# Performance work log

Hardware: AMD Instinct MI355X
Metric: run time of the kernel (lower is better)

The kernel has to match this reference:

```python
import jax, jax.numpy as jnp
import numpy as np

P = 16
IMG_SIZES = [(512, 512), (512, 384), (448, 512), (384, 384), (320, 448), (256, 512), (384, 256), (512, 320)]
LMAX = 1024
B, DIM, HEADS, DH, DEPTH, MLP, NC = 8, 512, 8, 64, 6, 2048, 1000
PD = 3 * P * P  # 768 patch dim


def layer_norm(x, w, b=None, eps=1e-5):
    mu = x.mean(-1, keepdims=True)
    var = ((x - mu) ** 2).mean(-1, keepdims=True)
    y = (x - mu) * jax.lax.rsqrt(var + eps) * w
    return y + b if b is not None else y


def _pack(images):
    # slice each image to its true (static) resolution, patchify, pad to LMAX
    toks, his, wis, msks = [], [], [], []
    for i, (H, W) in enumerate(IMG_SIZES):
        h, w = H // P, W // P
        L = h * w
        img = images[i, :, :H, :W]
        t = img.reshape(3, h, P, w, P).transpose(1, 3, 0, 2, 4).reshape(L, PD)
        hi = jnp.repeat(jnp.arange(h), w)
        wi = jnp.tile(jnp.arange(w), h)
        pad = LMAX - L
        toks.append(jnp.pad(t, ((0, pad), (0, 0))))
        his.append(jnp.pad(hi, (0, pad)))
        wis.append(jnp.pad(wi, (0, pad)))
        msks.append(jnp.arange(LMAX) < L)
    return jnp.stack(toks), jnp.stack(his), jnp.stack(wis), jnp.stack(msks)


def _mha(qx, kx, kmask, wq, wk, wv, qn, kn, wo):
    Bq, Lq, _ = qx.shape
    Lk = kx.shape[1]
    q = (qx @ wq.T).reshape(Bq, Lq, HEADS, DH)
    k = (kx @ wk.T).reshape(Bq, Lk, HEADS, DH)
    v = (kx @ wv.T).reshape(Bq, Lk, HEADS, DH)
    q = layer_norm(q, qn)
    k = layer_norm(k, kn)
    s = jnp.einsum('bqhd,bkhd->bhqk', q, k) / np.sqrt(DH).astype(np.float32)
    s = s + jnp.where(kmask[:, None, None, :], 0.0, -1e9)
    a = jax.nn.softmax(s, axis=-1)
    o = jnp.einsum('bhqk,bkhd->bqhd', a, v).reshape(Bq, Lq, HEADS * DH)
    return o @ wo.T


def setup_inputs() -> dict:
    key = jax.random.key(0)
    ks = iter(jax.random.split(key, 48))

    def nrm(shape, s=0.02):
        return jax.random.normal(next(ks), shape, jnp.float32) * s

    return {
        'images': jax.random.normal(next(ks), (B, 3, 512, 512), jnp.float32),
        'pe_ln1_w': jnp.ones(PD), 'pe_ln1_b': jnp.zeros(PD),
        'pe_w': nrm((DIM, PD)), 'pe_b': jnp.zeros(DIM),
        'pe_ln2_w': jnp.ones(DIM), 'pe_ln2_b': jnp.zeros(DIM),
        'pos_h': nrm((32, DIM), 1.0), 'pos_w': nrm((32, DIM), 1.0),
        'attn_ln': jnp.ones((DEPTH, DIM)),
        'wq': nrm((DEPTH, DIM, DIM)), 'wk': nrm((DEPTH, DIM, DIM)), 'wv': nrm((DEPTH, DIM, DIM)),
        'qn': jnp.ones((DEPTH, DH)), 'kn': jnp.ones((DEPTH, DH)),
        'wo': nrm((DEPTH, DIM, DIM)),
        'ff_ln': jnp.ones((DEPTH, DIM)),
        'ff_w1': nrm((DEPTH, MLP, DIM)), 'ff_b1': jnp.zeros((DEPTH, MLP)),
        'ff_w2': nrm((DEPTH, DIM, MLP)), 'ff_b2': jnp.zeros((DEPTH, DIM)),
        'final_ln': jnp.ones(DIM),
        'pool_q': nrm((DIM,), 1.0), 'pool_ln': jnp.ones(DIM),
        'pool_wq': nrm((DIM, DIM)), 'pool_wk': nrm((DIM, DIM)), 'pool_wv': nrm((DIM, DIM)),
        'pool_qn': jnp.ones(DH), 'pool_kn': jnp.ones(DH),
        'pool_wo': nrm((DIM, DIM)),
        'head_ln': jnp.ones(DIM), 'head_w': nrm((NC, DIM)),
    }


def reference(images, pe_ln1_w, pe_ln1_b, pe_w, pe_b, pe_ln2_w, pe_ln2_b, pos_h, pos_w,
              attn_ln, wq, wk, wv, qn, kn, wo, ff_ln, ff_w1, ff_b1, ff_w2, ff_b2,
              final_ln, pool_q, pool_ln, pool_wq, pool_wk, pool_wv, pool_qn, pool_kn,
              pool_wo, head_ln, head_w):
    tok, hi, wi, mask = _pack(images)
    t = layer_norm(tok, pe_ln1_w, pe_ln1_b)
    t = t @ pe_w.T + pe_b
    t = layer_norm(t, pe_ln2_w, pe_ln2_b)
    t = t + pos_h[hi] + pos_w[wi]
    t = t * mask[..., None]
    for l in range(DEPTH):
        xn = layer_norm(t, attn_ln[l])
        t = t + _mha(xn, xn, mask, wq[l], wk[l], wv[l], qn[l], kn[l], wo[l])
        h = layer_norm(t, ff_ln[l])
        t = t + (jax.nn.gelu(h @ ff_w1[l].T + ff_b1[l], approximate=False) @ ff_w2[l].T + ff_b2[l])
    t = layer_norm(t, final_ln)
    # attention pooling: one learned query per image; context = transformer output (unnormed inside attn)
    q = jnp.broadcast_to(pool_q, (B, 1, DIM))
    qn_ = layer_norm(q, pool_ln)
    pooled = _mha(qn_, t, mask, pool_wq, pool_wk, pool_wv, pool_qn, pool_kn, pool_wo)[:, 0]
    return layer_norm(pooled, head_ln) @ head_w.T
```

## Files before the change

### kernel.cpp

```cpp
#include <hip/hip_runtime.h>
#include <math.h>

#define LMAXS 1024
#define NB 8
#define DIM 512
#define HEADS 8
#define DH 64
#define DEPTH 6
#define MLP 2048
#define NC 1000
#define PDIM 768
#define MPACK 5376
#define MVALID 5360

typedef __attribute__((ext_vector_type(8))) short short8;
typedef __attribute__((ext_vector_type(4))) float floatx4;
typedef unsigned short ushort;

__constant__ int c_w[8]   = {32,24,32,24,28,32,16,20};
__constant__ int c_L[8]   = {1024,768,896,576,560,512,384,640};
__constant__ int c_off[9] = {0,1024,1792,2688,3264,3824,4336,4720,5360};

__device__ __forceinline__ int row2img(int r) {
  int b = 0;
  #pragma unroll
  for (int i = 1; i < 8; ++i) if (r >= c_off[i]) b = i;
  return b;
}

__device__ __forceinline__ ushort f2bf(float x) {
  unsigned int u = __float_as_uint(x);
  u += 0x7fff + ((u >> 16) & 1);
  return (ushort)(u >> 16);
}

#define GLOAD_LDS16(gp, lp) \
  __builtin_amdgcn_global_load_lds((const __attribute__((address_space(1))) void*)(gp), \
                                   (__attribute__((address_space(3))) void*)(lp), 16, 0, 0)

__device__ __forceinline__ void reduce2_256(float& s, float& s2, float* red) {
  #pragma unroll
  for (int off = 32; off; off >>= 1) {
    s  += __shfl_xor(s, off);
    s2 += __shfl_xor(s2, off);
  }
  int wv = threadIdx.x >> 6;
  if ((threadIdx.x & 63) == 0) { red[wv*2] = s; red[wv*2+1] = s2; }
  __syncthreads();
  s  = red[0] + red[2] + red[4] + red[6];
  s2 = red[1] + red[3] + red[5] + red[7];
  __syncthreads();
}

__global__ __launch_bounds__(256) void cvt_k(const float* __restrict__ s, ushort* __restrict__ d, int n) {
  int i = blockIdx.x*256 + threadIdx.x;
  if (i < n) d[i] = f2bf(s[i]);
}
__global__ __launch_bounds__(256) void cvt_qkv_k(
    const float* __restrict__ wq, const float* __restrict__ wk, const float* __restrict__ wv,
    ushort* __restrict__ d) {
  int i = blockIdx.x*256 + threadIdx.x;
  if (i >= 6*1536*512) return;
  int l = i / (1536*512), r = (i / 512) % 1536, k = i & 511;
  const float* src = (r < 512) ? wq : (r < 1024) ? wk : wv;
  int rr = r & 511;
  d[i] = f2bf(src[(size_t)l*DIM*DIM + (size_t)rr*DIM + k]);
}
__global__ __launch_bounds__(256) void cvt_pool_k(
    const float* __restrict__ wk, const float* __restrict__ wv, ushort* __restrict__ d) {
  int i = blockIdx.x*256 + threadIdx.x;
  if (i >= 1024*512) return;
  int r = i >> 9, k = i & 511;
  d[i] = f2bf(r < 512 ? wk[(size_t)r*DIM + k] : wv[(size_t)(r-512)*DIM + k]);
}

__global__ __launch_bounds__(256) void pack_ln1_k(
    const float* __restrict__ images, const float* __restrict__ g,
    const float* __restrict__ bb, ushort* __restrict__ tok) {
  int r = blockIdx.x;
  ushort* out = tok + (size_t)r * PDIM;
  if (r >= MVALID) {
    for (int i = threadIdx.x; i < PDIM; i += 256) out[i] = 0;
    return;
  }
  int b = row2img(r), l = r - c_off[b];
  int wgrid = c_w[b];
  __shared__ float vals[PDIM];
  __shared__ float red[8];
  int hp = l / wgrid, wp = l % wgrid;
  const float* base = images + (size_t)b*3*512*512 + (size_t)hp*16*512 + wp*16;
  float s = 0.f, s2 = 0.f;
  for (int i = threadIdx.x; i < PDIM; i += 256) {
    int c = i >> 8, rr = (i >> 4) & 15, cc = i & 15;
    float v = base[(size_t)c*512*512 + rr*512 + cc];
    vals[i] = v; s += v; s2 += v*v;
  }
  reduce2_256(s, s2, red);
  float mu = s * (1.f/PDIM);
  float rs = rsqrtf(fmaxf(s2*(1.f/PDIM) - mu*mu, 0.f) + 1e-5f);
  for (int i = threadIdx.x; i < PDIM; i += 256)
    out[i] = f2bf((vals[i]-mu)*rs*g[i] + bb[i]);
}

template<int ACT, int OUT>
__global__ __launch_bounds__(256) void gemm_bf(
    const ushort* __restrict__ A, const ushort* __restrict__ W,
    const float* __restrict__ bias, void* __restrict__ Cv,
    int M, int N, int K) {
  __shared__ ushort As[128*64];
  __shared__ ushort Ws[128*64];
  int tid = threadIdx.x;
  int row0 = blockIdx.y*128, col0 = blockIdx.x*128;
  int lane = tid & 63, l15 = lane & 15, quad = lane >> 4;
  int wv = tid >> 6, wm = wv >> 1, wn = wv & 1;
  int sw = l15 & 7;
  int segA = (quad ^ sw) * 8, segB = segA ^ 32;
  const ushort *Ap[4], *Wp[4];
  #pragma unroll
  for (int j = 0; j < 4; ++j) {
    int blk = j*256 + tid;
    int r = blk >> 3, s = ((blk & 7) ^ (r & 7)) * 8;
    Ap[j] = A + (size_t)(row0 + r)*K + s;
    Wp[j] = W + (size_t)(col0 + r)*K + s;
  }
  int ksl = K / gridDim.z;
  int kb0 = blockIdx.z * ksl;
  floatx4 acc[4][4] = {};
  for (int k0 = kb0; k0 < kb0 + ksl; k0 += 64) {
    __syncthreads();
    #pragma unroll
    for (int j = 0; j < 4; ++j) {
      GLOAD_LDS16(Ap[j] + k0, &As[(j*256+tid)*8]);
      GLOAD_LDS16(Wp[j] + k0, &Ws[(j*256+tid)*8]);
    }
    __syncthreads();
    #pragma unroll
    for (int w = 0; w < 2; ++w) {
      int sg = w ? segB : segA;
      short8 af[4], bf[4];
      #pragma unroll
      for (int i = 0; i < 4; ++i) af[i] = *(const short8*)&As[(wm*64 + i*16 + l15)*64 + sg];
      #pragma unroll
      for (int j = 0; j < 4; ++j) bf[j] = *(const short8*)&Ws[(wn*64 + j*16 + l15)*64 + sg];
      #pragma unroll
      for (int i = 0; i < 4; ++i)
        #pragma unroll
        for (int j = 0; j < 4; ++j)
          acc[i][j] = __builtin_amdgcn_mfma_f32_16x16x32_bf16(af[i], bf[j], acc[i][j], 0, 0, 0);
    }
  }
  int rb = row0 + wm*64 + quad*4;
  int cb = col0 + wn*64 + l15;
  bool addb = (bias != nullptr) && (blockIdx.z == 0);
  float* outz = (float*)Cv + (OUT == 3 ? (size_t)blockIdx.z * M * N : 0);
  #pragma unroll
  for (int j = 0; j < 4; ++j) {
    int cc = cb + j*16;
    float bsum = addb ? bias[cc] : 0.f;
    #pragma unroll
    for (int i = 0; i < 4; ++i) {
      int rr = rb + i*16;
      #pragma unroll
      for (int reg = 0; reg < 4; ++reg) {
        float v = acc[i][j][reg] + bsum;
        if (ACT == 1) v = 0.5f*v*(1.f + erff(v*0.70710678118654752f));
        size_t idx = (size_t)(rr + reg)*N + cc;
        if (OUT == 0)      ((float*)Cv)[idx] = v;
        else if (OUT == 1) ((float*)Cv)[idx] += v;
        else if (OUT == 3) outz[idx] = v;
        else               ((ushort*)Cv)[idx] = f2bf(v);
      }
    }
  }
}

template<int POOL>
__global__ __launch_bounds__(256) void gemm_qkv_k(
    const ushort* __restrict__ A, const ushort* __restrict__ W,
    const float* __restrict__ gq, const float* __restrict__ gk,
    ushort* __restrict__ Qh, ushort* __restrict__ Kh, ushort* __restrict__ Vh,
    float* __restrict__ KV, int N) {
  const int K = DIM;
  __shared__ ushort As[128*64];
  __shared__ ushort Ws[128*64];
  int tid = threadIdx.x;
  int row0 = blockIdx.y*128, col0 = blockIdx.x*128;
  int lane = tid & 63, l15 = lane & 15, quad = lane >> 4;
  int wv = tid >> 6, wm = wv >> 1, wn = wv & 1;
  int sw = l15 & 7;
  int segA = (quad ^ sw) * 8, segB = segA ^ 32;
  const ushort *Ap[4], *Wp[4];
  #pragma unroll
  for (int j = 0; j < 4; ++j) {
    int blk = j*256 + tid;
    int r = blk >> 3, s = ((blk & 7) ^ (r & 7)) * 8;
    Ap[j] = A + (size_t)(row0 + r)*K + s;
    Wp[j] = W + (size_t)(col0 + r)*K + s;
  }
  floatx4 acc[4][4] = {};
  for (int k0 = 0; k0 < K; k0 += 64) {
    __syncthreads();
    #pragma unroll
    for (int j = 0; j < 4; ++j) {
      GLOAD_LDS16(Ap[j] + k0, &As[(j*256+tid)*8]);
      GLOAD_LDS16(Wp[j] + k0, &Ws[(j*256+tid)*8]);
    }
    __syncthreads();
    #pragma unroll
    for (int w = 0; w < 2; ++w) {
      int sg = w ? segB : segA;
      short8 af[4], bf[4];
      #pragma unroll
      for (int i = 0; i < 4; ++i) af[i] = *(const short8*)&As[(wm*64 + i*16 + l15)*64 + sg];
      #pragma unroll
      for (int j = 0; j < 4; ++j) bf[j] = *(const short8*)&Ws[(wn*64 + j*16 + l15)*64 + sg];
      #pragma unroll
      for (int i = 0; i < 4; ++i)
        #pragma unroll
        for (int j = 0; j < 4; ++j)
          acc[i][j] = __builtin_amdgcn_mfma_f32_16x16x32_bf16(af[i], bf[j], acc[i][j], 0, 0, 0);
    }
  }
  int unit = (col0 >> 6) + wn;
  bool needln = POOL ? (unit < 8) : (unit < 16);
  const float* gain = POOL ? gq : (unit < 8 ? gq : gk);
  #pragma unroll
  for (int i = 0; i < 4; ++i) {
    float s[4] = {0,0,0,0}, s2[4] = {0,0,0,0};
    if (needln) {
      #pragma unroll
      for (int j = 0; j < 4; ++j)
        #pragma unroll
        for (int reg = 0; reg < 4; ++reg) {
          float v = acc[i][j][reg];
          s[reg] += v; s2[reg] += v*v;
        }
      #pragma unroll
      for (int reg = 0; reg < 4; ++reg)
        #pragma unroll
        for (int off = 1; off < 16; off <<= 1) {
          s[reg]  += __shfl_xor(s[reg],  off);
          s2[reg] += __shfl_xor(s2[reg], off);
        }
    }
    #pragma unroll
    for (int reg = 0; reg < 4; ++reg) {
      int r = row0 + wm*64 + i*16 + quad*4 + reg;
      if (r >= MVALID) continue;
      float mu = s[reg]*(1.f/64.f);
      float rs = rsqrtf(fmaxf(s2[reg]*(1.f/64.f) - mu*mu, 0.f) + 1e-5f);
      int b = row2img(r), l = r - c_off[b];
      #pragma unroll
      for (int j = 0; j < 4; ++j) {
        int dh = j*16 + l15;
        float v = acc[i][j][reg];
        if (needln) v = (v - mu)*rs*gain[dh];
        if (POOL) {
          KV[(size_t)r*1024 + unit*64 + dh] = v;
        } else {
          int h = unit & 7;
          size_t dst = ((size_t)(b*8+h)*LMAXS + l)*64 + dh;
          if (unit < 8)       Qh[dst] = f2bf(v);
          else if (unit < 16) Kh[dst] = f2bf(v);
          else                Vh[dst] = f2bf(v);
        }
      }
    }
  }
}

__global__ __launch_bounds__(256) void row_ln_add2_k(
    float* __restrict__ T, const float* __restrict__ P0, const float* __restrict__ P1,
    const float* __restrict__ g, ushort* __restrict__ Y) {
  __shared__ float red[8];
  size_t base = (size_t)blockIdx.x * DIM;
  float v0 = T[base + threadIdx.x], v1 = T[base + threadIdx.x + 256];
  if (P0) {
    v0 += P0[base + threadIdx.x] + P1[base + threadIdx.x];
    v1 += P0[base + threadIdx.x + 256] + P1[base + threadIdx.x + 256];
    T[base + threadIdx.x] = v0;
    T[base + threadIdx.x + 256] = v1;
  }
  float s = v0 + v1, s2 = v0*v0 + v1*v1;
  reduce2_256(s, s2, red);
  float mu = s*(1.f/DIM), rs = rsqrtf(fmaxf(s2*(1.f/DIM) - mu*mu, 0.f) + 1e-5f);
  Y[base + threadIdx.x]       = f2bf((v0-mu)*rs*g[threadIdx.x]);
  Y[base + threadIdx.x + 256] = f2bf((v1-mu)*rs*g[threadIdx.x + 256]);
}

__global__ __launch_bounds__(256) void ln2_pos_k(
    float* __restrict__ T, const float* __restrict__ g, const float* __restrict__ bb,
    const float* __restrict__ ph, const float* __restrict__ pw) {
  int r = blockIdx.x;
  float* x = T + (size_t)r * DIM;
  if (r >= MVALID) {
    for (int i = threadIdx.x; i < DIM; i += 256) x[i] = 0.f;
    return;
  }
  int b = row2img(r), l = r - c_off[b];
  __shared__ float red[8];
  int wgrid = c_w[b];
  int hi = l / wgrid, wi = l % wgrid;
  float s=0.f, s2=0.f;
  for (int i = threadIdx.x; i < DIM; i += 256) { float v = x[i]; s+=v; s2+=v*v; }
  reduce2_256(s, s2, red);
  float mu = s*(1.f/DIM), rs = rsqrtf(fmaxf(s2*(1.f/DIM)-mu*mu, 0.f)+1e-5f);
  for (int i = threadIdx.x; i < DIM; i += 256)
    x[i] = (x[i]-mu)*rs*g[i] + bb[i] + ph[hi*DIM+i] + pw[wi*DIM+i];
}

__global__ __launch_bounds__(256) void vtrans_k(
    const ushort* __restrict__ Vh, ushort* __restrict__ VhT) {
  int bh = blockIdx.x, b = bh >> 3;
  int lt = blockIdx.y;
  if (lt*64 >= c_L[b]) return;
  __shared__ ushort t[64][72];
  int tid = threadIdx.x;
  int row = tid >> 2, seg = (tid & 3)*16;
  const ushort* src = Vh + ((size_t)bh*LMAXS + lt*64 + row)*64 + seg;
  *(short8*)&t[row][seg]   = *(const short8*)src;
  *(short8*)&t[row][seg+8] = *(const short8*)(src+8);
  __syncthreads();
  int dh = tid >> 2, ks = (tid & 3)*16;
  short8 o0, o1;
  #pragma unroll
  for (int jj = 0; jj < 8; ++jj) o0[jj] = (short)t[ks+jj][dh];
  #pragma unroll
  for (int jj = 0; jj < 8; ++jj) o1[jj] = (short)t[ks+8+jj][dh];
  ushort* dst = VhT + ((size_t)bh*64 + dh)*LMAXS + lt*64 + ks;
  *(short8*)dst     = o0;
  *(short8*)(dst+8) = o1;
}

__global__ __launch_bounds__(256) void attn_mfma_k(
    const ushort* __restrict__ Qh, const ushort* __restrict__ Kh,
    const ushort* __restrict__ VhT, ushort* __restrict__ O) {
  int bh = blockIdx.x, b = bh >> 3, h = bh & 7;
  int Lb = c_L[b];
  int qt = blockIdx.y;
  if (qt * 64 >= Lb) return;
  __shared__ ushort Ks[64*64];
  __shared__ ushort Vt[64*64];
  __shared__ ushort Pb[4][16][68];
  int tid = threadIdx.x, wv = tid >> 6, lane = tid & 63;
  int quad = lane >> 4, l15 = lane & 15;
  int sw = l15 & 7;
  int segA = (quad ^ sw) * 8, segB = segA ^ 32;
  int q0 = qt*64 + wv*16;
  bool active = q0 < Lb;
  const ushort* qhb = Qh + (size_t)bh * LMAXS * DH;
  const ushort* khb = Kh + (size_t)bh * LMAXS * DH;
  const ushort* vtb = VhT + (size_t)bh * DH * LMAXS;
  short8 aq0 = {}, aq1 = {};
  if (active) {
    const ushort* qp = qhb + (size_t)(q0 + l15) * DH;
    aq0 = *(const short8*)(qp + quad*8);
    aq1 = *(const short8*)(qp + 32 + quad*8);
  }
  int blk0 = tid, blk1 = tid + 256;
  int kr0 = blk0 >> 3, s0 = ((blk0 & 7) ^ (kr0 & 7)) * 8;
  int kr1 = blk1 >> 3, s1 = ((blk1 & 7) ^ (kr1 & 7)) * 8;
  const ushort* kg0 = khb + kr0*DH + s0;
  const ushort* kg1 = khb + kr1*DH + s1;
  const ushort* vg0 = vtb + (size_t)kr0*LMAXS + s0;
  const ushort* vg1 = vtb + (size_t)kr1*LMAXS + s1;
  float lsum[4] = {0.f,0.f,0.f,0.f};
  floatx4 o[4] = {};
  for (int kc = 0; kc < Lb; kc += 64) {
    __syncthreads();
    GLOAD_LDS16(kg0 + kc*DH, &Ks[blk0*8]);
    GLOAD_LDS16(kg1 + kc*DH, &Ks[blk1*8]);
    GLOAD_LDS16(vg0 + kc,    &Vt[blk0*8]);
    GLOAD_LDS16(vg1 + kc,    &Vt[blk1*8]);
    __syncthreads();
    if (!active) continue;
    bool tail = (kc + 64 > Lb);
    #pragma unroll
    for (int kb = 0; kb < 4; ++kb) {
      int krow = (kb*16 + l15) * 64;
      floatx4 s = {};
      s = __builtin_amdgcn_mfma_f32_16x16x32_bf16(aq0, *(const short8*)&Ks[krow + segA], s, 0,0,0);
      s = __builtin_amdgcn_mfma_f32_16x16x32_bf16(aq1, *(const short8*)&Ks[krow + segB], s, 0,0,0);
      #pragma unroll
      for (int reg = 0; reg < 4; ++reg) {
        float x = s[reg] * 0.125f;
        if (tail && (kc + kb*16 + l15 >= Lb)) x = -1e9f;
        float p = __expf(x);
        lsum[reg] += p;
        Pb[wv][quad*4+reg][kb*16+l15] = f2bf(p);
      }
    }
    short8 a0 = *(const short8*)&Pb[wv][l15][quad*8];
    short8 a1 = *(const short8*)&Pb[wv][l15][32+quad*8];
    #pragma unroll
    for (int nb = 0; nb < 4; ++nb) {
      int vrow = (nb*16 + l15) * 64;
      o[nb] = __builtin_amdgcn_mfma_f32_16x16x32_bf16(a0, *(const short8*)&Vt[vrow + segA], o[nb], 0,0,0);
      o[nb] = __builtin_amdgcn_mfma_f32_16x16x32_bf16(a1, *(const short8*)&Vt[vrow + segB], o[nb], 0,0,0);
    }
  }
  if (active) {
    float inv[4];
    #pragma unroll
    for (int reg = 0; reg < 4; ++reg) {
      float s = lsum[reg];
      s += __shfl_xor(s,1); s += __shfl_xor(s,2); s += __shfl_xor(s,4); s += __shfl_xor(s,8);
      inv[reg] = 1.f / s;
    }
    int rbase = c_off[b] + q0 + quad*4;
    #pragma unroll
    for (int nb = 0; nb < 4; ++nb)
      #pragma unroll
      for (int reg = 0; reg < 4; ++reg)
        O[(size_t)(rbase+reg)*DIM + h*DH + nb*16 + l15] = f2bf(o[nb][reg] * inv[reg]);
  }
}

__global__ __launch_bounds__(256) void pool_prep_a_k(
    const float* __restrict__ pq, const float* __restrict__ pln,
    const float* __restrict__ pwq, float* __restrict__ qp) {
  __shared__ float qln[DIM];
  __shared__ float red[8];
  int tid = threadIdx.x;
  float s=0.f, s2=0.f;
  for (int i=tid;i<DIM;i+=256){ float v=pq[i]; s+=v; s2+=v*v; }
  reduce2_256(s, s2, red);
  float mu=s*(1.f/DIM), rs=rsqrtf(fmaxf(s2*(1.f/DIM)-mu*mu,0.f)+1e-5f);
  for (int i=tid;i<DIM;i+=256) qln[i]=(pq[i]-mu)*rs*pln[i];
  __syncthreads();
  int n = blockIdx.x*64 + (tid>>2);
  int kq = (tid&3)*128;
  const float4* wr = (const float4*)(pwq + (size_t)n*DIM + kq);
  float a=0.f;
  #pragma unroll
  for (int k=0;k<32;++k) {
    float4 w4 = wr[k];
    float4 q4 = *(const float4*)&qln[kq + k*4];
    a += w4.x*q4.x + w4.y*q4.y + w4.z*q4.z + w4.w*q4.w;
  }
  a += __shfl_xor(a,1); a += __shfl_xor(a,2);
  if ((tid&3)==0) qp[n]=a;
}

__global__ __launch_bounds__(512) void pool_prep_b_k(
    const float* __restrict__ qp, const float* __restrict__ pqn, float* __restrict__ qpool) {
  int h = threadIdx.x >> 6, lane = threadIdx.x & 63;
  float v = qp[h*64 + lane];
  float s = v, s2 = v*v;
  #pragma unroll
  for (int off=32; off; off>>=1) { s += __shfl_xor(s,off); s2 += __shfl_xor(s2,off); }
  float mu = s*(1.f/64), rs = rsqrtf(fmaxf(s2*(1.f/64)-mu*mu, 0.f)+1e-5f);
  qpool[h*64+lane] = (v-mu)*rs*pqn[lane];
}

__global__ __launch_bounds__(256) void pool_attn_part_k(
    const float* __restrict__ qpool, const float* __restrict__ KV,
    float* __restrict__ PART) {
  __shared__ float qh[DH];
  __shared__ float ps[256];
  __shared__ float op[4][DH];
  __shared__ float red[8];
  int bh = blockIdx.x, c = blockIdx.y;
  int b = bh>>3, h = bh&7;
  int Lb = c_L[b];
  int tid = threadIdx.x;
  if (tid < DH) qh[tid] = qpool[h*DH + tid];
  __syncthreads();
  int kk = c*256 + tid;
  float p = 0.f;
  if (kk < Lb) {
    const float4* kp = (const float4*)(KV + (size_t)(c_off[b]+kk)*1024 + h*DH);
    float a = 0.f;
    #pragma unroll
    for (int dd=0; dd<16; ++dd) {
      float4 kv = kp[dd];
      a += kv.x*qh[dd*4] + kv.y*qh[dd*4+1] + kv.z*qh[dd*4+2] + kv.w*qh[dd*4+3];
    }
    p = __expf(a*0.125f);
  }
  ps[tid] = p;
  float s = p, s2 = 0.f;
  reduce2_256(s, s2, red);
  int wvv = tid >> 6, lane = tid & 63;
  float o = 0.f;
  int kb = c*256 + wvv*64;
  const float* vb = KV + (size_t)c_off[b]*1024 + 512 + h*DH + lane;
  for (int j = 0; j < 64; ++j) {
    int key = kb + j;
    if (key < Lb) o += ps[wvv*64+j] * vb[(size_t)key*1024];
  }
  op[wvv][lane] = o;
  __syncthreads();
  if (tid < DH)
    PART[((size_t)bh*4 + c)*66 + tid] = op[0][tid]+op[1][tid]+op[2][tid]+op[3][tid];
  if (tid == 64)
    PART[((size_t)bh*4 + c)*66 + 64] = s;
}

__global__ __launch_bounds__(64) void pool_attn_comb_k(
    const float* __restrict__ PART, float* __restrict__ O) {
  int bh = blockIdx.x, b = bh>>3, h = bh&7, d = threadIdx.x;
  float o = 0.f, sum = 0.f;
  #pragma unroll
  for (int c = 0; c < 4; ++c) {
    o   += PART[((size_t)bh*4 + c)*66 + d];
    sum += PART[((size_t)bh*4 + c)*66 + 64];
  }
  O[(size_t)b*DIM + h*DH + d] = o / sum;
}

__global__ __launch_bounds__(256) void proj512_k(
    const float* __restrict__ X, const float* __restrict__ W, float* __restrict__ Y) {
  __shared__ float xr[DIM];
  int b = blockIdx.x, tid = threadIdx.x;
  for (int i=tid;i<DIM;i+=256) xr[i] = X[(size_t)b*DIM+i];
  __syncthreads();
  if (tid < 128) {
    int n = blockIdx.y*128 + tid;
    const float4* wr = (const float4*)(W + (size_t)n*DIM);
    float a=0.f;
    for (int k=0;k<DIM/4;++k) { float4 w4 = wr[k]; a += w4.x*xr[k*4]+w4.y*xr[k*4+1]+w4.z*xr[k*4+2]+w4.w*xr[k*4+3]; }
    Y[(size_t)b*DIM+n]=a;
  }
}

__global__ __launch_bounds__(256) void head_out_k(
    const float* __restrict__ X, const float* __restrict__ g,
    const float* __restrict__ W, float* __restrict__ out) {
  __shared__ float xr[DIM];
  __shared__ float red[8];
  int b = blockIdx.x, tid = threadIdx.x;
  float s=0.f, s2=0.f;
  for (int i=tid;i<DIM;i+=256){ float v=X[(size_t)b*DIM+i]; s+=v; s2+=v*v; }
  reduce2_256(s, s2, red);
  float mu=s*(1.f/DIM), rs=rsqrtf(fmaxf(s2*(1.f/DIM)-mu*mu,0.f)+1e-5f);
  for (int i=tid;i<DIM;i+=256) xr[i]=(X[(size_t)b*DIM+i]-mu)*rs*g[i];
  __syncthreads();
  if (tid < 125) {
    int n = blockIdx.y*125 + tid;
    const float4* wr = (const float4*)(W + (size_t)n*DIM);
    float a=0.f;
    for (int k=0;k<DIM/4;++k){ float4 w4=wr[k]; a += w4.x*xr[k*4]+w4.y*xr[k*4+1]+w4.z*xr[k*4+2]+w4.w*xr[k*4+3]; }
    out[(size_t)b*NC+n]=a;
  }
}

extern "C" void kernel_launch(void* const* d_in, const int* in_sizes, int n_in,
                              void* d_out, int out_size, void* d_ws, size_t ws_size,
                              hipStream_t stream) {
  const float* images  = (const float*)d_in[0];
  const float* pe_ln1_w= (const float*)d_in[1];
  const float* pe_ln1_b= (const float*)d_in[2];
  const float* pe_w    = (const float*)d_in[3];
  const float* pe_b    = (const float*)d_in[4];
  const float* pe_ln2_w= (const float*)d_in[5];
  const float* pe_ln2_b= (const float*)d_in[6];
  const float* pos_h   = (const float*)d_in[7];
  const float* pos_w   = (const float*)d_in[8];
  const float* attn_ln = (const float*)d_in[9];
  const float* wq      = (const float*)d_in[10];
  const float* wk      = (const float*)d_in[11];
  const float* wvp     = (const float*)d_in[12];
  const float* qn      = (const float*)d_in[13];
  const float* kn      = (const float*)d_in[14];
  const float* wo      = (const float*)d_in[15];
  const float* ff_ln   = (const float*)d_in[16];
  const float* ff_w1   = (const float*)d_in[17];
  const float* ff_b1   = (const float*)d_in[18];
  const float* ff_w2   = (const float*)d_in[19];
  const float* ff_b2   = (const float*)d_in[20];
  const float* final_ln= (const float*)d_in[21];
  const float* pool_q  = (const float*)d_in[22];
  const float* pool_ln = (const float*)d_in[23];
  const float* pool_wq = (const float*)d_in[24];
  const float* pool_wk = (const float*)d_in[25];
  const float* pool_wv = (const float*)d_in[26];
  const float* pool_qn = (const float*)d_in[27];
  const float* pool_kn = (const float*)d_in[28];
  const float* pool_wo = (const float*)d_in[29];
  const float* head_ln = (const float*)d_in[30];
  const float* head_w  = (const float*)d_in[31];
  (void)ws_size; (void)in_sizes; (void)n_in; (void)out_size;

  char* p = (char*)d_ws;
  ushort* WQKVc = (ushort*)p; p += (size_t)6*1536*512*2;
  ushort* WOc   = (ushort*)p; p += (size_t)6*512*512*2;
  ushort* W1c   = (ushort*)p; p += (size_t)6*2048*512*2;
  ushort* W2c   = (ushort*)p; p += (size_t)6*512*2048*2;
  ushort* PEWc  = (ushort*)p; p += (size_t)512*768*2;
  ushort* PKVc  = (ushort*)p; p += (size_t)1024*512*2;
  float*  T     = (float*)p;  p += (size_t)MPACK*DIM*4;
  ushort* XN    = (ushort*)p; p += (size_t)MPACK*DIM*2;
  float*  KVb   = (float*)p;  p += (size_t)MPACK*1024*4;
  float*  P0    = KVb;
  float*  P1    = KVb + (size_t)MPACK*DIM;
  ushort* Qh    = (ushort*)p; p += (size_t)64*LMAXS*DH*2;
  ushort* Kh    = (ushort*)p; p += (size_t)64*LMAXS*DH*2;
  ushort* Vh    = (ushort*)p; p += (size_t)64*LMAXS*DH*2;
  ushort* VhT   = (ushort*)p; p += (size_t)64*64*LMAXS*2;
  ushort* FFH   = (ushort*)p; p += (size_t)MPACK*MLP*2;
  ushort* TOK   = FFH;
  ushort* ATTO  = FFH;
  float*  QP    = (float*)p;  p += DIM*4;
  float*  QPOOL = (float*)p;  p += DIM*4;
  float*  POOLO = (float*)p;  p += NB*DIM*4;
  float*  POOLED= (float*)p;  p += NB*DIM*4;
  float*  PART  = (float*)p;  p += (size_t)64*4*66*4;

  cvt_qkv_k<<<(6*1536*512+255)/256, 256, 0, stream>>>(wq, wk, wvp, WQKVc);
  cvt_k<<<(6*512*512+255)/256, 256, 0, stream>>>(wo, WOc, 6*512*512);
  cvt_k<<<(6*2048*512+255)/256, 256, 0, stream>>>(ff_w1, W1c, 6*2048*512);
  cvt_k<<<(6*512*2048+255)/256, 256, 0, stream>>>(ff_w2, W2c, 6*512*2048);
  cvt_k<<<(512*768+255)/256, 256, 0, stream>>>(pe_w, PEWc, 512*768);
  cvt_pool_k<<<(1024*512+255)/256, 256, 0, stream>>>(pool_wk, pool_wv, PKVc);

  pack_ln1_k<<<MPACK, 256, 0, stream>>>(images, pe_ln1_w, pe_ln1_b, TOK);
  gemm_bf<0,0><<<dim3(4, MPACK/128), 256, 0, stream>>>(TOK, PEWc, pe_b, T, MPACK, DIM, PDIM);
  ln2_pos_k<<<MPACK, 256, 0, stream>>>(T, pe_ln2_w, pe_ln2_b, pos_h, pos_w);

  for (int l = 0; l < DEPTH; ++l) {
    row_ln_add2_k<<<MPACK, 256, 0, stream>>>(T, l ? P0 : nullptr, P1, attn_ln + l*DIM, XN);
    gemm_qkv_k<0><<<dim3(12, MPACK/128), 256, 0, stream>>>(
        XN, WQKVc + (size_t)l*1536*512, qn + l*DH, kn + l*DH, Qh, Kh, Vh, nullptr, 1536);
    vtrans_k<<<dim3(64, 16), 256, 0, stream>>>(Vh, VhT);
    attn_mfma_k<<<dim3(64, 16), 256, 0, stream>>>(Qh, Kh, VhT, ATTO);
    gemm_bf<0,3><<<dim3(4, MPACK/128, 2), 256, 0, stream>>>(ATTO, WOc + (size_t)l*512*512, nullptr, P0, MPACK, DIM, DIM);
    row_ln_add2_k<<<MPACK, 256, 0, stream>>>(T, P0, P1, ff_ln + l*DIM, XN);
    gemm_bf<1,2><<<dim3(16, MPACK/128), 256, 0, stream>>>(XN, W1c + (size_t)l*MLP*DIM, ff_b1 + l*MLP, FFH, MPACK, MLP, DIM);
    gemm_bf<0,3><<<dim3(4, MPACK/128, 2), 256, 0, stream>>>(FFH, W2c + (size_t)l*DIM*MLP, ff_b2 + l*DIM, P0, MPACK, DIM, MLP);
  }

  row_ln_add2_k<<<MPACK, 256, 0, stream>>>(T, P0, P1, final_ln, XN);
  pool_prep_a_k<<<8, 256, 0, stream>>>(pool_q, pool_ln, pool_wq, QP);
  pool_prep_b_k<<<1, 512, 0, stream>>>(QP, pool_qn, QPOOL);
  gemm_qkv_k<1><<<dim3(8, MPACK/128), 256, 0, stream>>>(
      XN, PKVc, pool_kn, nullptr, nullptr, nullptr, nullptr, KVb, 1024);
  pool_attn_part_k<<<dim3(64, 4), 256, 0, stream>>>(QPOOL, KVb, PART);
  pool_attn_comb_k<<<64, 64, 0, stream>>>(PART, POOLO);
  proj512_k<<<dim3(8, 4), 256, 0, stream>>>(POOLO, pool_wo, POOLED);
  head_out_k<<<dim3(8, 8), 256, 0, stream>>>(POOLED, head_ln, head_w, (float*)d_out);
}
```

Before: 1.265 ms.

## Split attention over key slices with a separate combine kernel

The attention kernel now splits each query tile's key range into 256-key slices across a third grid dimension and writes unnormalized partial outputs and row sums. A new combine kernel adds the slices and normalizes into the bf16 output. The softmax scale and log2(e) are folded into Q at QKV projection time so the inner loop can use exp2. The workspace is reorganized to alias the partial buffer with dead buffers. The aim is more parallelism for long sequences, at the cost of extra partial-buffer traffic and an extra launch.

```diff
diff --git a/kernel.cpp b/kernel.cpp
--- a/kernel.cpp
+++ b/kernel.cpp
@@ -12,6 +12,7 @@
 #define PDIM 768
 #define MPACK 5376
 #define MVALID 5360
+#define QSCALE 0.18033688f
 
 typedef __attribute__((ext_vector_type(8))) short short8;
 typedef __attribute__((ext_vector_type(4))) float floatx4;
@@ -166,7 +167,6 @@
         if (ACT == 1) v = 0.5f*v*(1.f + erff(v*0.70710678118654752f));
         size_t idx = (size_t)(rr + reg)*N + cc;
         if (OUT == 0)      ((float*)Cv)[idx] = v;
-        else if (OUT == 1) ((float*)Cv)[idx] += v;
         else if (OUT == 3) outz[idx] = v;
         else               ((ushort*)Cv)[idx] = f2bf(v);
       }
@@ -260,7 +260,7 @@
         } else {
           int h = unit & 7;
           size_t dst = ((size_t)(b*8+h)*LMAXS + l)*64 + dh;
-          if (unit < 8)       Qh[dst] = f2bf(v);
+          if (unit < 8)       Qh[dst] = f2bf(v * QSCALE);
           else if (unit < 16) Kh[dst] = f2bf(v);
           else                Vh[dst] = f2bf(v);
         }
@@ -312,14 +312,21 @@
 __global__ __launch_bounds__(256) void vtrans_k(
     const ushort* __restrict__ Vh, ushort* __restrict__ VhT) {
   int bh = blockIdx.x, b = bh >> 3;
+  int Lb = c_L[b];
   int lt = blockIdx.y;
-  if (lt*64 >= c_L[b]) return;
+  if (lt*64 >= Lb) return;
   __shared__ ushort t[64][72];
   int tid = threadIdx.x;
   int row = tid >> 2, seg = (tid & 3)*16;
-  const ushort* src = Vh + ((size_t)bh*LMAXS + lt*64 + row)*64 + seg;
-  *(short8*)&t[row][seg]   = *(const short8*)src;
-  *(short8*)&t[row][seg+8] = *(const short8*)(src+8);
+  short8 z8 = {};
+  if (lt*64 + row < Lb) {
+    const ushort* src = Vh + ((size_t)bh*LMAXS + lt*64 + row)*64 + seg;
+    *(short8*)&t[row][seg]   = *(const short8*)src;
+    *(short8*)&t[row][seg+8] = *(const short8*)(src+8);
+  } else {
+    *(short8*)&t[row][seg]   = z8;
+    *(short8*)&t[row][seg+8] = z8;
+  }
   __syncthreads();
   int dh = tid >> 2, ks = (tid & 3)*16;
   short8 o0, o1;
@@ -332,13 +339,13 @@
   *(short8*)(dst+8) = o1;
 }
 
-__global__ __launch_bounds__(256) void attn_mfma_k(
+__global__ __launch_bounds__(256) void attn_part_k(
     const ushort* __restrict__ Qh, const ushort* __restrict__ Kh,
-    const ushort* __restrict__ VhT, ushort* __restrict__ O) {
-  int bh = blockIdx.x, b = bh >> 3, h = bh & 7;
+    const ushort* __restrict__ VhT, float* __restrict__ PART) {
+  int bh = blockIdx.x, b = bh >> 3;
   int Lb = c_L[b];
-  int qt = blockIdx.y;
-  if (qt * 64 >= Lb) return;
+  int qt = blockIdx.y, z = blockIdx.z;
+  if (qt*64 >= Lb || z*256 >= Lb) return;
   __shared__ ushort Ks[64*64];
   __shared__ ushort Vt[64*64];
   __shared__ ushort Pb[4][16][68];
@@ -364,9 +371,10 @@
   const ushort* kg1 = khb + kr1*DH + s1;
   const ushort* vg0 = vtb + (size_t)kr0*LMAXS + s0;
   const ushort* vg1 = vtb + (size_t)kr1*LMAXS + s1;
+  int kbeg = z*256, kend = min(kbeg + 256, Lb);
   float lsum[4] = {0.f,0.f,0.f,0.f};
   floatx4 o[4] = {};
-  for (int kc = 0; kc < Lb; kc += 64) {
+  for (int kc = kbeg; kc < kend; kc += 64) {
     __syncthreads();
     GLOAD_LDS16(kg0 + kc*DH, &Ks[blk0*8]);
     GLOAD_LDS16(kg1 + kc*DH, &Ks[blk1*8]);
@@ -383,9 +391,9 @@
       s = __builtin_amdgcn_mfma_f32_16x16x32_bf16(aq1, *(const short8*)&Ks[krow + segB], s, 0,0,0);
       #pragma unroll
       for (int reg = 0; reg < 4; ++reg) {
-        float x = s[reg] * 0.125f;
+        float x = s[reg];
         if (tail && (kc + kb*16 + l15 >= Lb)) x = -1e9f;
-        float p = __expf(x);
+        float p = __builtin_amdgcn_exp2f(x);
         lsum[reg] += p;
         Pb[wv][quad*4+reg][kb*16+l15] = f2bf(p);
       }
@@ -400,20 +408,54 @@
     }
   }
   if (active) {
-    float inv[4];
+    size_t sb = ((size_t)(bh*16 + qt)*4 + z) * 4160;
     #pragma unroll
     for (int reg = 0; reg < 4; ++reg) {
       float s = lsum[reg];
       s += __shfl_xor(s,1); s += __shfl_xor(s,2); s += __shfl_xor(s,4); s += __shfl_xor(s,8);
-      inv[reg] = 1.f / s;
-    }
-    int rbase = c_off[b] + q0 + quad*4;
+      if (l15 == 0) PART[sb + 4096 + wv*16 + quad*4 + reg] = s;
+    }
+    int rq = wv*16 + quad*4;
     #pragma unroll
     for (int nb = 0; nb < 4; ++nb)
       #pragma unroll
       for (int reg = 0; reg < 4; ++reg)
-        O[(size_t)(rbase+reg)*DIM + h*DH + nb*16 + l15] = f2bf(o[nb][reg] * inv[reg]);
-  }
+        PART[sb + (size_t)(rq + reg)*64 + nb*16 + l15] = o[nb][reg];
+  }
+}
+
+__global__ __launch_bounds__(256) void attn_comb_k(
+    const float* __restrict__ PART, ushort* __restrict__ O) {
+  int bh = blockIdx.x, b = bh >> 3, h = bh & 7;
+  int Lb = c_L[b];
+  int qt = blockIdx.y;
+  if (qt*64 >= Lb) return;
+  int nsl = (Lb + 255) >> 8;
+  int t = threadIdx.x;
+  int q = t >> 2, dj = (t & 3) * 16;
+  int qq = qt*64 + q;
+  if (qq >= Lb) return;
+  size_t base = (size_t)(bh*16 + qt)*4*4160;
+  float o[16] = {};
+  float l = 0.f;
+  for (int zz = 0; zz < nsl; ++zz) {
+    const float* sp = PART + base + (size_t)zz*4160;
+    #pragma unroll
+    for (int i = 0; i < 16; i += 4) {
+      float4 v = *(const float4*)&sp[q*64 + dj + i];
+      o[i] += v.x; o[i+1] += v.y; o[i+2] += v.z; o[i+3] += v.w;
+    }
+    l += sp[4096 + q];
+  }
+  float inv = 1.f / l;
+  short8 r0, r1;
+  #pragma unroll
+  for (int i = 0; i < 8; ++i) r0[i] = (short)f2bf(o[i]*inv);
+  #pragma unroll
+  for (int i = 0; i < 8; ++i) r1[i] = (short)f2bf(o[8+i]*inv);
+  ushort* dst = O + (size_t)(c_off[b]+qq)*DIM + h*DH + dj;
+  *(short8*)dst     = r0;
+  *(short8*)(dst+8) = r1;
 }
 
 __global__ __launch_bounds__(256) void pool_prep_a_k(
@@ -455,7 +497,7 @@
 
 __global__ __launch_bounds__(256) void pool_attn_part_k(
     const float* __restrict__ qpool, const float* __restrict__ KV,
-    float* __restrict__ PART) {
+    float* __restrict__ PARTP) {
   __shared__ float qh[DH];
   __shared__ float ps[256];
   __shared__ float op[4][DH];
@@ -492,19 +534,19 @@
   op[wvv][lane] = o;
   __syncthreads();
   if (tid < DH)
-    PART[((size_t)bh*4 + c)*66 + tid] = op[0][tid]+op[1][tid]+op[2][tid]+op[3][tid];
+    PARTP[((size_t)bh*4 + c)*66 + tid] = op[0][tid]+op[1][tid]+op[2][tid]+op[3][tid];
   if (tid == 64)
-    PART[((size_t)bh*4 + c)*66 + 64] = s;
+    PARTP[((size_t)bh*4 + c)*66 + 64] = s;
 }
 
 __global__ __launch_bounds__(64) void pool_attn_comb_k(
-    const float* __restrict__ PART, float* __restrict__ O) {
+    const float* __restrict__ PARTP, float* __restrict__ O) {
   int bh = blockIdx.x, b = bh>>3, h = bh&7, d = threadIdx.x;
   float o = 0.f, sum = 0.f;
   #pragma unroll
   for (int c = 0; c < 4; ++c) {
-    o   += PART[((size_t)bh*4 + c)*66 + d];
-    sum += PART[((size_t)bh*4 + c)*66 + 64];
+    o   += PARTP[((size_t)bh*4 + c)*66 + d];
+    sum += PARTP[((size_t)bh*4 + c)*66 + 64];
   }
   O[(size_t)b*DIM + h*DH + d] = o / sum;
 }
@@ -590,22 +632,24 @@
   ushort* PEWc  = (ushort*)p; p += (size_t)512*768*2;
   ushort* PKVc  = (ushort*)p; p += (size_t)1024*512*2;
   float*  T     = (float*)p;  p += (size_t)MPACK*DIM*4;
-  ushort* XN    = (ushort*)p; p += (size_t)MPACK*DIM*2;
-  float*  KVb   = (float*)p;  p += (size_t)MPACK*1024*4;
-  float*  P0    = KVb;
-  float*  P1    = KVb + (size_t)MPACK*DIM;
   ushort* Qh    = (ushort*)p; p += (size_t)64*LMAXS*DH*2;
   ushort* Kh    = (ushort*)p; p += (size_t)64*LMAXS*DH*2;
-  ushort* Vh    = (ushort*)p; p += (size_t)64*LMAXS*DH*2;
   ushort* VhT   = (ushort*)p; p += (size_t)64*64*LMAXS*2;
   ushort* FFH   = (ushort*)p; p += (size_t)MPACK*MLP*2;
   ushort* TOK   = FFH;
   ushort* ATTO  = FFH;
+  char*   R     = p;          p += (size_t)64*16*4*4160*4;
+  float*  PART  = (float*)R;
+  float*  P0    = (float*)R;
+  float*  P1    = (float*)(R + (size_t)MPACK*DIM*4);
+  ushort* XN    = (ushort*)(R + (size_t)2*MPACK*DIM*4);
+  ushort* Vh    = (ushort*)(R + (size_t)2*MPACK*DIM*4 + (size_t)MPACK*DIM*2);
+  float*  KVb   = (float*)R;
   float*  QP    = (float*)p;  p += DIM*4;
   float*  QPOOL = (float*)p;  p += DIM*4;
   float*  POOLO = (float*)p;  p += NB*DIM*4;
   float*  POOLED= (float*)p;  p += NB*DIM*4;
-  float*  PART  = (float*)p;  p += (size_t)64*4*66*4;
+  float*  PARTP = (float*)p;  p += (size_t)64*4*66*4;
 
   cvt_qkv_k<<<(6*1536*512+255)/256, 256, 0, stream>>>(wq, wk, wvp, WQKVc);
   cvt_k<<<(6*512*512+255)/256, 256, 0, stream>>>(wo, WOc, 6*512*512);
@@ -623,7 +667,8 @@
     gemm_qkv_k<0><<<dim3(12, MPACK/128), 256, 0, stream>>>(
         XN, WQKVc + (size_t)l*1536*512, qn + l*DH, kn + l*DH, Qh, Kh, Vh, nullptr, 1536);
     vtrans_k<<<dim3(64, 16), 256, 0, stream>>>(Vh, VhT);
-    attn_mfma_k<<<dim3(64, 16), 256, 0, stream>>>(Qh, Kh, VhT, ATTO);
+    attn_part_k<<<dim3(64, 16, 4), 256, 0, stream>>>(Qh, Kh, VhT, PART);
+    attn_comb_k<<<dim3(64, 16), 256, 0, stream>>>(PART, ATTO);
     gemm_bf<0,3><<<dim3(4, MPACK/128, 2), 256, 0, stream>>>(ATTO, WOc + (size_t)l*512*512, nullptr, P0, MPACK, DIM, DIM);
     row_ln_add2_k<<<MPACK, 256, 0, stream>>>(T, P0, P1, ff_ln + l*DIM, XN);
     gemm_bf<1,2><<<dim3(16, MPACK/128), 256, 0, stream>>>(XN, W1c + (size_t)l*MLP*DIM, ff_b1 + l*MLP, FFH, MPACK, MLP, DIM);
@@ -635,8 +680,8 @@
   pool_prep_b_k<<<1, 512, 0, stream>>>(QP, pool_qn, QPOOL);
   gemm_qkv_k<1><<<dim3(8, MPACK/128), 256, 0, stream>>>(
       XN, PKVc, pool_kn, nullptr, nullptr, nullptr, nullptr, KVb, 1024);
-  pool_attn_part_k<<<dim3(64, 4), 256, 0, stream>>>(QPOOL, KVb, PART);
-  pool_attn_comb_k<<<64, 64, 0, stream>>>(PART, POOLO);
+  pool_attn_part_k<<<dim3(64, 4), 256, 0, stream>>>(QPOOL, KVb, PARTP);
+  pool_attn_comb_k<<<64, 64, 0, stream>>>(PARTP, POOLO);
   proj512_k<<<dim3(8, 4), 256, 0, stream>>>(POOLO, pool_wo, POOLED);
   head_out_k<<<dim3(8, 8), 256, 0, stream>>>(POOLED, head_ln, head_w, (float*)d_out);
 }
```

Result: slower. 1.293 ms (+2.2%).
